# Optimization experiments

Hardware: AMD Instinct MI355X
Metric: run time of the kernel (lower is better)

The kernel has to match this reference:

```python
import jax, jax.numpy as jnp
import numpy as np

H = 1024      # hidden_size
NH = 16       # num_attention_heads
HD = H // NH  # head_size
DF = 4096     # ff intermediate
EPS = 1e-5


def layer_norm(x, g, b):
    mu = jnp.mean(x, axis=-1, keepdims=True)
    var = jnp.var(x, axis=-1, keepdims=True)
    return (x - mu) * jax.lax.rsqrt(var + EPS) * g + b


def setup_inputs() -> dict:
    key = jax.random.key(0)
    ks = jax.random.split(key, 4)
    s = 0.02
    return {
        "x": jax.random.normal(ks[0], (2, 2048, H), dtype=jnp.float32),
        "w_qkv": jax.random.normal(ks[1], (H, 3 * H), dtype=jnp.float32) * s,
        "ln1_g": jnp.ones((H,), jnp.float32),
        "ln1_b": jnp.zeros((H,), jnp.float32),
        "w1": jax.random.normal(ks[2], (H, DF), dtype=jnp.float32) * s,
        "b1": jnp.zeros((DF,), jnp.float32),
        "w2": jax.random.normal(ks[3], (DF, H), dtype=jnp.float32) * s,
        "b2": jnp.zeros((H,), jnp.float32),
        "ln2_g": jnp.ones((H,), jnp.float32),
        "ln2_b": jnp.zeros((H,), jnp.float32),
    }


def reference(x, w_qkv, ln1_g, ln1_b, w1, b1, w2, b2, ln2_g, ln2_b):
    b, s, h = x.shape
    # --- MHSelfAttention (naive) ---
    qkv = x @ w_qkv                                   # [b, s, 3h]
    qkv = qkv.reshape(b, s, 3, NH, HD)
    q, k, v = (jnp.moveaxis(qkv, 2, 0)                # [3, b, s, nh, hd]
               .transpose(0, 1, 3, 2, 4))             # [3, b, nh, s, hd]
    # NOTE: faithful quirk — scaled by sqrt(hidden_size), not head_size
    scores = jnp.einsum('bnqd,bnkd->bnqk', q, k) / jnp.sqrt(jnp.float32(h))
    probs = jax.nn.softmax(scores, axis=-1)
    ctx = jnp.einsum('bnqk,bnkd->bnqd', probs, v)     # [b, nh, s, hd]
    attn_out = ctx.transpose(0, 2, 1, 3).reshape(b, s, h)
    # post-norm residual (dropout = identity in eval)
    x = x + layer_norm(attn_out, ln1_g, ln1_b)
    # --- FFN ---
    ff = jax.nn.relu(x @ w1 + b1) @ w2 + b2
    x = x + layer_norm(ff, ln2_g, ln2_b)
    return x
```

## Files before the change

### kernel.cpp

```cpp
#include <hip/hip_runtime.h>


typedef unsigned short u16;
typedef unsigned int u32;
typedef __bf16 bf16x8 __attribute__((ext_vector_type(8)));
typedef float f32x4 __attribute__((ext_vector_type(4)));
typedef float f32x16 __attribute__((ext_vector_type(16)));
typedef u32 u32x4 __attribute__((ext_vector_type(4)));
typedef u16 u16x4 __attribute__((ext_vector_type(4)));

__device__ __forceinline__ u16 f2b(float f) {
  u32 u = __builtin_bit_cast(u32, f);
  u += 0x7fffu + ((u >> 16) & 1u);
  return (u16)(u >> 16);
}
__device__ __forceinline__ float b2f(u16 u) {
  return __builtin_bit_cast(float, (u32)u << 16);
}

__device__ __forceinline__ u32 cvtpk(float lo, float hi) {
  u32 r;
  asm("v_cvt_pk_bf16_f32 %0, %1, %2" : "=v"(r) : "v"(lo), "v"(hi));
  return r;
}

__device__ __forceinline__ void gld_lds16(const u16* g, u16* l) {
  __builtin_amdgcn_global_load_lds(
      (const __attribute__((address_space(1))) u32*)g,
      (__attribute__((address_space(3))) u32*)l, 16, 0, 0);
}

__device__ __forceinline__ void transpose32(
    const float* __restrict__ in, u16* __restrict__ out, int R, int C,
    int bx, int by, float (*tile)[33], int tid) {
  const int cb = bx * 32, rb = by * 32;
  const int c = tid & 31;
  const int r0 = tid >> 5;
#pragma unroll
  for (int rr = 0; rr < 32; rr += 8)
    tile[r0 + rr][c] = in[(size_t)(rb + r0 + rr) * C + cb + c];
  __syncthreads();
#pragma unroll
  for (int rr = 0; rr < 32; rr += 8)
    out[(size_t)(cb + r0 + rr) * R + rb + c] = f2b(tile[c][r0 + rr]);
}

__global__ __launch_bounds__(256) void prep1_kernel(
    const float* __restrict__ x, u16* __restrict__ xb,
    const float* __restrict__ w_qkv, u16* __restrict__ wqkvT) {
  __shared__ float tile[32][33];
  const int bid = blockIdx.x;
  const int tid = threadIdx.x;
  if (bid < 4096) {
    const int idx = bid * 256 + tid;
    float4 v = ((const float4*)x)[idx];
    u16x4 o = { f2b(v.x), f2b(v.y), f2b(v.z), f2b(v.w) };
    ((u16x4*)xb)[idx] = o;
  } else {
    const int t = bid - 4096;
    transpose32(w_qkv, wqkvT, 1024, 3072, t % 96, t / 96, tile, tid);
  }
}

__global__ __launch_bounds__(256) void prep2_kernel(
    const float* __restrict__ w1, u16* __restrict__ w1T,
    const float* __restrict__ w2, u16* __restrict__ w2T) {
  __shared__ float tile[32][33];
  const int bid = blockIdx.x;
  const int tid = threadIdx.x;
  if (bid < 4096) {
    transpose32(w1, w1T, 1024, 4096, bid % 128, bid / 128, tile, tid);
  } else {
    const int t = bid - 4096;
    transpose32(w2, w2T, 4096, 1024, t % 32, t / 32, tile, tid);
  }
}

__global__ __launch_bounds__(256) void transpose_v_kernel(
    const u16* __restrict__ qkv, u16* __restrict__ vt) {
  __shared__ u16 t[64][70];
  const int bh = blockIdx.x, st = blockIdx.y;
  const int b = bh >> 4, nh = bh & 15;
  const int s0 = st * 64;
  const int r = threadIdx.x >> 3, c = (threadIdx.x & 7) << 3;
  const u16* src = qkv + (size_t)(b * 2048 + s0) * 3072 + 2048 + nh * 64;
#pragma unroll
  for (int rr = 0; rr < 64; rr += 32)
    *(u32x4*)&t[r + rr][c] = *(const u32x4*)(src + (size_t)(r + rr) * 3072 + c);
  __syncthreads();
  u16* dst = vt + ((size_t)bh * 64) * 2048 + s0;
#pragma unroll
  for (int rr = 0; rr < 64; rr += 32) {
    const int d = r + rr;
    u16 tmp[8];
#pragma unroll
    for (int j = 0; j < 8; ++j) tmp[j] = t[c + j][d];
    *(u32x4*)(dst + (size_t)d * 2048 + c) = *(u32x4*)tmp;
  }
}

#define GT16(BUF, SBUF, T2, VM)                                               \
  {                                                                           \
    const u16(*Ab)[32] = As[BUF];                                             \
    const u16(*Bb)[32] = Bs[BUF];                                             \
    bf16x8 af[4], bfr[4];                                                     \
    _Pragma("unroll") for (int nr = 0; nr < 4; ++nr)                          \
        bfr[nr] = *(const bf16x8*)&Bb[wn * 64 + nr * 16 + l16][cRd];          \
    _Pragma("unroll") for (int mr = 0; mr < 4; ++mr)                          \
        af[mr] = *(const bf16x8*)&Ab[wm * 64 + mr * 16 + l16][cRd];           \
    if ((T2) >= 0) {                                                          \
      gld_lds16(Ag + (size_t)(T2) * 32, &As[SBUF][w * 16][0]);                \
      gld_lds16(Bg + (size_t)(T2) * 32, &Bs[SBUF][w * 16][0]);                \
    }                                                                         \
    asm volatile("s_waitcnt lgkmcnt(0)" ::: "memory");                        \
    __builtin_amdgcn_sched_barrier(0);                                        \
    __builtin_amdgcn_s_setprio(1);                                            \
    _Pragma("unroll") for (int mr = 0; mr < 4; ++mr)                          \
        _Pragma("unroll") for (int nr = 0; nr < 4; ++nr)                      \
            acc[mr][nr] = __builtin_amdgcn_mfma_f32_16x16x32_bf16(            \
                af[mr], bfr[nr], acc[mr][nr], 0, 0, 0);                       \
    __builtin_amdgcn_s_setprio(0);                                            \
    if ((VM) == 2) asm volatile("s_waitcnt vmcnt(2)" ::: "memory");           \
    else if ((VM) == 0) asm volatile("s_waitcnt vmcnt(0)" ::: "memory");      \
    if ((VM) >= 0) __builtin_amdgcn_s_barrier();                              \
  }

__global__ __launch_bounds__(1024) void gemm256_kernel(
    const u16* __restrict__ A, const u16* __restrict__ Bt,
    const float* __restrict__ bias, u16* __restrict__ Cb,
    int M, int N, int K, int relu,
    u16* __restrict__ Cb1, u16* __restrict__ Cb2, u16* __restrict__ Cb3) {
  const int nN = N >> 8;
  const int lin = (blockIdx.x & 7) * ((int)gridDim.x >> 3) + (blockIdx.x >> 3);
  const int m0 = (lin / nN) << 8;
  const int n0 = (lin % nN) << 8;
  const int z = blockIdx.y;
  if (z == 1) Cb = Cb1; else if (z == 2) Cb = Cb2; else if (z == 3) Cb = Cb3;

  const int tid = threadIdx.x;
  const int w = tid >> 6, lane = tid & 63;
  const int quad = lane >> 4, l16 = lane & 15;
  const int wm = w >> 2, wn = w & 3;

  __shared__ u16 As[3][256][32];
  __shared__ u16 Bs[3][256][32];

  f32x4 acc[4][4];
#pragma unroll
  for (int i = 0; i < 4; ++i)
#pragma unroll
    for (int j = 0; j < 4; ++j) acc[i][j] = {0.f, 0.f, 0.f, 0.f};

  const int srow = lane >> 2;
  const int scol = (((lane & 3) ^ (srow & 3)) << 3);
  const u16* Ag = A + (size_t)(m0 + w * 16 + srow) * K + (size_t)z * 1024 + scol;
  const u16* Bg = Bt + (size_t)(n0 + w * 16 + srow) * K + (size_t)z * 1024 + scol;

  const int cRd = ((quad ^ (l16 & 3)) << 3);

  gld_lds16(Ag,      &As[0][w * 16][0]);
  gld_lds16(Bg,      &Bs[0][w * 16][0]);
  gld_lds16(Ag + 32, &As[1][w * 16][0]);
  gld_lds16(Bg + 32, &Bs[1][w * 16][0]);
  asm volatile("s_waitcnt vmcnt(2)" ::: "memory");
  __builtin_amdgcn_s_barrier();

  for (int tt = 0; tt < 10; ++tt) {
    const int t = tt * 3;
    GT16(0, 2, t + 2, 2)
    GT16(1, 0, t + 3, 2)
    GT16(2, 1, t + 4, 2)
  }
  GT16(0, 0, -1, 0)
  GT16(1, 0, -1, -1)

#pragma unroll
  for (int mr = 0; mr < 4; ++mr) {
    const int row = m0 + wm * 64 + mr * 16 + quad * 4;
#pragma unroll
    for (int nr = 0; nr < 4; ++nr) {
      const int col = n0 + wn * 64 + nr * 16 + l16;
      const float bv = bias ? bias[col] : 0.f;
#pragma unroll
      for (int r = 0; r < 4; ++r) {
        float v = acc[mr][nr][r] + bv;
        if (relu) v = fmaxf(v, 0.f);
        Cb[(size_t)(row + r) * N + col] = f2b(v);
      }
    }
  }
}

#define QVMC                                                                  \
  if (w < 12) { asm volatile("s_waitcnt vmcnt(2)" ::: "memory"); }            \
  else        { asm volatile("s_waitcnt vmcnt(1)" ::: "memory"); }
#define QGT16(BUF, SBUF, T2, VM)                                              \
  {                                                                           \
    const u16(*Ab)[32] = As[BUF];                                             \
    const u16(*Bb)[32] = Bs[BUF];                                             \
    bf16x8 af[4], bfr[3];                                                     \
    _Pragma("unroll") for (int nr = 0; nr < 3; ++nr)                          \
        bfr[nr] = *(const bf16x8*)&Bb[wn * 48 + nr * 16 + l16][cRd];          \
    _Pragma("unroll") for (int mr = 0; mr < 4; ++mr)                          \
        af[mr] = *(const bf16x8*)&Ab[wm * 64 + mr * 16 + l16][cRd];           \
    if ((T2) >= 0) {                                                          \
      gld_lds16(Ag + (size_t)(T2) * 32, &As[SBUF][w * 16][0]);                \
      if (w < 12)                                                             \
        gld_lds16(Bg + (size_t)(T2) * 32, &Bs[SBUF][w * 16][0]);              \
    }                                                                         \
    asm volatile("s_waitcnt lgkmcnt(0)" ::: "memory");                        \
    __builtin_amdgcn_sched_barrier(0);                                        \
    __builtin_amdgcn_s_setprio(1);                                            \
    _Pragma("unroll") for (int mr = 0; mr < 4; ++mr)                          \
        _Pragma("unroll") for (int nr = 0; nr < 3; ++nr)                      \
            acc[mr][nr] = __builtin_amdgcn_mfma_f32_16x16x32_bf16(            \
                af[mr], bfr[nr], acc[mr][nr], 0, 0, 0);                       \
    __builtin_amdgcn_s_setprio(0);                                            \
    if ((VM) == 2) { QVMC }                                                   \
    else if ((VM) == 0) asm volatile("s_waitcnt vmcnt(0)" ::: "memory");      \
    if ((VM) >= 0) __builtin_amdgcn_s_barrier();                              \
  }

__global__ __launch_bounds__(1024) void gemm_qkv_kernel(
    const u16* __restrict__ A, const u16* __restrict__ Bt,
    u16* __restrict__ Cb) {
  const int K = 1024, N = 3072;
  const int lin = (blockIdx.x & 7) * 32 + (blockIdx.x >> 3);
  const int m0 = (lin >> 4) << 8;
  const int n0 = (lin & 15) * 192;

  const int tid = threadIdx.x;
  const int w = tid >> 6, lane = tid & 63;
  const int quad = lane >> 4, l16 = lane & 15;
  const int wm = w >> 2, wn = w & 3;

  __shared__ u16 As[3][256][32];
  __shared__ u16 Bs[3][192][32];

  f32x4 acc[4][3];
#pragma unroll
  for (int i = 0; i < 4; ++i)
#pragma unroll
    for (int j = 0; j < 3; ++j) acc[i][j] = {0.f, 0.f, 0.f, 0.f};

  const int srow = lane >> 2;
  const int scol = (((lane & 3) ^ (srow & 3)) << 3);
  const u16* Ag = A + (size_t)(m0 + w * 16 + srow) * K + scol;
  const u16* Bg = Bt + (size_t)(n0 + w * 16 + srow) * K + scol;

  const int cRd = ((quad ^ (l16 & 3)) << 3);

  gld_lds16(Ag,      &As[0][w * 16][0]);
  if (w < 12) gld_lds16(Bg,      &Bs[0][w * 16][0]);
  gld_lds16(Ag + 32, &As[1][w * 16][0]);
  if (w < 12) gld_lds16(Bg + 32, &Bs[1][w * 16][0]);
  QVMC
  __builtin_amdgcn_s_barrier();

  for (int tt = 0; tt < 10; ++tt) {
    const int t = tt * 3;
    QGT16(0, 2, t + 2, 2)
    QGT16(1, 0, t + 3, 2)
    QGT16(2, 1, t + 4, 2)
  }
  QGT16(0, 0, -1, 0)
  QGT16(1, 0, -1, -1)

#pragma unroll
  for (int mr = 0; mr < 4; ++mr) {
    const int row = m0 + wm * 64 + mr * 16 + quad * 4;
#pragma unroll
    for (int nr = 0; nr < 3; ++nr) {
      const int col = n0 + wn * 48 + nr * 16 + l16;
#pragma unroll
      for (int r = 0; r < 4; ++r)
        Cb[(size_t)(row + r) * N + col] = f2b(acc[mr][nr][r]);
    }
  }
}

__global__ __launch_bounds__(256, 4) void attn_kernel(
    const u16* __restrict__ qkv, const u16* __restrict__ vt,
    float* __restrict__ Op0, float* __restrict__ Op1,
    float* __restrict__ lpart) {
  const int bh = blockIdx.x;
  const int qt = blockIdx.y;
  const int kz = blockIdx.z;
  const int b = bh >> 4, nh = bh & 15;
  const int tid = threadIdx.x;
  const int w = tid >> 6, lane = tid & 63;
  const int l32 = lane & 31, hi = lane >> 5;
  const float c2 = 0.04508422f;

  __shared__ u16 KS[64][64];
  __shared__ u16 VS[64][64];

  const size_t rs = 3072;
  const u16* qbase = qkv + (size_t)b * 2048 * rs + nh * 64;
  const u16* kbase = qbase + 1024;
  const u16* vbase = vt + (size_t)bh * 64 * 2048;
  const int q0 = qt * 128;
  const int k0beg = kz * 1024;

  bf16x8 aq[4];
  {
    const u16* qrow = qbase + (size_t)(q0 + w * 32 + l32) * rs + hi * 8;
#pragma unroll
    for (int ds = 0; ds < 4; ++ds) {
      u32x4 v = *(const u32x4*)(qrow + ds * 16);
      u16 ti[8], to[8];
      *(u32x4*)ti = v;
#pragma unroll
      for (int j = 0; j < 8; ++j) to[j] = f2b(b2f(ti[j]) * c2);
      u32x4 pk = *(u32x4*)to;
      aq[ds] = __builtin_bit_cast(bf16x8, pk);
    }
  }

  f32x16 Oacc[2];
#pragma unroll
  for (int dn = 0; dn < 2; ++dn)
#pragma unroll
    for (int i = 0; i < 16; ++i) Oacc[dn][i] = 0.f;
  float ls[4] = {0.f, 0.f, 0.f, 0.f};

  const int srow = lane >> 3;
  const int scol = ((lane & 7) ^ srow) << 3;

#pragma unroll 1
  for (int t = 0; t < 16; ++t) {
    const int k0 = k0beg + t * 64;
    __syncthreads();
    gld_lds16(kbase + (size_t)(k0 + w * 16 + srow) * rs + scol,       &KS[w * 16][0]);
    gld_lds16(kbase + (size_t)(k0 + w * 16 + 8 + srow) * rs + scol,   &KS[w * 16 + 8][0]);
    gld_lds16(vbase + (size_t)(w * 16 + srow) * 2048 + k0 + scol,     &VS[w * 16][0]);
    gld_lds16(vbase + (size_t)(w * 16 + 8 + srow) * 2048 + k0 + scol, &VS[w * 16 + 8][0]);
    __syncthreads();

    f32x16 S[2];
#pragma unroll
    for (int jt = 0; jt < 2; ++jt)
#pragma unroll
      for (int i = 0; i < 16; ++i) S[jt][i] = 0.f;
#pragma unroll
    for (int jt = 0; jt < 2; ++jt) {
      const int krow = jt * 32 + l32;
#pragma unroll
      for (int ds = 0; ds < 4; ++ds) {
        bf16x8 kv = *(const bf16x8*)&KS[krow][((2 * ds + hi) ^ (krow & 7)) << 3];
        S[jt] = __builtin_amdgcn_mfma_f32_32x32x16_bf16(kv, aq[ds], S[jt], 0, 0, 0);
      }
    }

    bf16x8 pa[4];
#pragma unroll
    for (int jt = 0; jt < 2; ++jt) {
      float p[16];
#pragma unroll
      for (int r = 0; r < 16; ++r) {
        p[r] = exp2f(S[jt][r]);
        ls[r & 3] += p[r];
      }
#pragma unroll
      for (int bq = 0; bq < 2; ++bq) {
        u32 x0 = cvtpk(p[8 * bq + 0], p[8 * bq + 1]);
        u32 y0 = cvtpk(p[8 * bq + 4], p[8 * bq + 5]);
        u32 x1 = cvtpk(p[8 * bq + 2], p[8 * bq + 3]);
        u32 y1 = cvtpk(p[8 * bq + 6], p[8 * bq + 7]);
        asm("v_permlane32_swap_b32 %0, %1" : "+v"(x0), "+v"(y0));
        asm("v_permlane32_swap_b32 %0, %1" : "+v"(x1), "+v"(y1));
        u32x4 dw = {x0, x1, y0, y1};
        pa[2 * jt + bq] = __builtin_bit_cast(bf16x8, dw);
      }
    }

#pragma unroll
    for (int dn = 0; dn < 2; ++dn) {
      const int vrow = dn * 32 + l32;
#pragma unroll
      for (int ks = 0; ks < 4; ++ks) {
        bf16x8 vv = *(const bf16x8*)&VS[vrow][((2 * ks + hi) ^ (vrow & 7)) << 3];
        Oacc[dn] = __builtin_amdgcn_mfma_f32_32x32x16_bf16(pa[ks], vv, Oacc[dn], 0, 0, 0);
      }
    }
  }

  float lsum = (ls[0] + ls[1]) + (ls[2] + ls[3]);
  const float ltot = lsum + __shfl_xor(lsum, 32);

  float* opart = kz ? Op1 : Op0;
  float* obase = opart + (size_t)b * 2048 * 1024 + (size_t)nh * 64;
  float* lbase = lpart + (size_t)kz * 4096 * 16 + (size_t)b * 2048 * 16 + nh;
#pragma unroll
  for (int r = 0; r < 16; ++r) {
    const int qrow = q0 + w * 32 + (r & 3) + 8 * (r >> 2) + 4 * hi;
#pragma unroll
    for (int dn = 0; dn < 2; ++dn)
      obase[(size_t)qrow * 1024 + dn * 32 + l32] = Oacc[dn][r];
  }
  if (lane < 32) lbase[(size_t)(q0 + w * 32 + l32) * 16] = ltot;
}

__global__ __launch_bounds__(256) void ln_attn_kernel(
    const float* __restrict__ O0, const float* __restrict__ O1,
    const float* __restrict__ l0, const float* __restrict__ l1,
    const float* __restrict__ xres, const float* __restrict__ g,
    const float* __restrict__ bb, float* __restrict__ outf,
    u16* __restrict__ outb) {
  const int w = threadIdx.x >> 6, lane = threadIdx.x & 63;
  const int row = blockIdx.x * 4 + w;
  const float4* o0r = (const float4*)(O0 + (size_t)row * 1024);
  const float4* o1r = (const float4*)(O1 + (size_t)row * 1024);
  const float* lp0 = l0 + row * 16;
  const float* lp1 = l1 + row * 16;

  float4 v[4];
  float s = 0.f, s2 = 0.f;
#pragma unroll
  for (int j = 0; j < 4; ++j) {
    const int f = j * 64 + lane;
    const int head = f >> 4;
    const float inv = 1.f / (lp0[head] + lp1[head]);
    float4 a0 = o0r[f];
    float4 a1 = o1r[f];
    v[j].x = (a0.x + a1.x) * inv;
    v[j].y = (a0.y + a1.y) * inv;
    v[j].z = (a0.z + a1.z) * inv;
    v[j].w = (a0.w + a1.w) * inv;
    s  += v[j].x + v[j].y + v[j].z + v[j].w;
    s2 += v[j].x * v[j].x + v[j].y * v[j].y + v[j].z * v[j].z + v[j].w * v[j].w;
  }
#pragma unroll
  for (int off = 32; off > 0; off >>= 1) {
    s += __shfl_xor(s, off);
    s2 += __shfl_xor(s2, off);
  }
  const float mu = s * (1.f / 1024.f);
  const float var = s2 * (1.f / 1024.f) - mu * mu;
  const float rstd = rsqrtf(var + 1e-5f);

  const float4* xr4 = (const float4*)(xres + (size_t)row * 1024);
  float4* of4 = (float4*)(outf + (size_t)row * 1024);
  u16x4* ob4 = (u16x4*)(outb + (size_t)row * 1024);
#pragma unroll
  for (int j = 0; j < 4; ++j) {
    const int f = j * 64 + lane;
    float4 xr = xr4[f];
    float4 gv = ((const float4*)g)[f];
    float4 bv = ((const float4*)bb)[f];
    float4 o;
    o.x = xr.x + (v[j].x - mu) * rstd * gv.x + bv.x;
    o.y = xr.y + (v[j].y - mu) * rstd * gv.y + bv.y;
    o.z = xr.z + (v[j].z - mu) * rstd * gv.z + bv.z;
    o.w = xr.w + (v[j].w - mu) * rstd * gv.w + bv.w;
    of4[f] = o;
    u16x4 ob = { f2b(o.x), f2b(o.y), f2b(o.z), f2b(o.w) };
    ob4[f] = ob;
  }
}

__global__ __launch_bounds__(256) void ln_ffn_kernel(
    const u16* __restrict__ p0, const u16* __restrict__ p1,
    const u16* __restrict__ p2, const u16* __restrict__ p3,
    const float* __restrict__ bias, const float* __restrict__ xres,
    const float* __restrict__ g, const float* __restrict__ bb,
    float* __restrict__ outf) {
  const int w = threadIdx.x >> 6, lane = threadIdx.x & 63;
  const int row = blockIdx.x * 4 + w;
  const u16x4* p0r = (const u16x4*)(p0 + (size_t)row * 1024);
  const u16x4* p1r = (const u16x4*)(p1 + (size_t)row * 1024);
  const u16x4* p2r = (const u16x4*)(p2 + (size_t)row * 1024);
  const u16x4* p3r = (const u16x4*)(p3 + (size_t)row * 1024);

  float4 v[4];
  float s = 0.f, s2 = 0.f;
#pragma unroll
  for (int j = 0; j < 4; ++j) {
    const int f = j * 64 + lane;
    u16x4 a0 = p0r[f];
    u16x4 a1 = p1r[f];
    u16x4 a2 = p2r[f];
    u16x4 a3 = p3r[f];
    float4 bv4 = ((const float4*)bias)[f];
    v[j].x = (b2f(a0[0]) + b2f(a1[0])) + (b2f(a2[0]) + b2f(a3[0])) + bv4.x;
    v[j].y = (b2f(a0[1]) + b2f(a1[1])) + (b2f(a2[1]) + b2f(a3[1])) + bv4.y;
    v[j].z = (b2f(a0[2]) + b2f(a1[2])) + (b2f(a2[2]) + b2f(a3[2])) + bv4.z;
    v[j].w = (b2f(a0[3]) + b2f(a1[3])) + (b2f(a2[3]) + b2f(a3[3])) + bv4.w;
    s  += v[j].x + v[j].y + v[j].z + v[j].w;
    s2 += v[j].x * v[j].x + v[j].y * v[j].y + v[j].z * v[j].z + v[j].w * v[j].w;
  }
#pragma unroll
  for (int off = 32; off > 0; off >>= 1) {
    s += __shfl_xor(s, off);
    s2 += __shfl_xor(s2, off);
  }
  const float mu = s * (1.f / 1024.f);
  const float var = s2 * (1.f / 1024.f) - mu * mu;
  const float rstd = rsqrtf(var + 1e-5f);

  const float4* xr4 = (const float4*)(xres + (size_t)row * 1024);
  float4* of4 = (float4*)(outf + (size_t)row * 1024);
#pragma unroll
  for (int j = 0; j < 4; ++j) {
    const int f = j * 64 + lane;
    float4 xr = xr4[f];
    float4 gv = ((const float4*)g)[f];
    float4 bv = ((const float4*)bb)[f];
    float4 o;
    o.x = xr.x + (v[j].x - mu) * rstd * gv.x + bv.x;
    o.y = xr.y + (v[j].y - mu) * rstd * gv.y + bv.y;
    o.z = xr.z + (v[j].z - mu) * rstd * gv.z + bv.z;
    o.w = xr.w + (v[j].w - mu) * rstd * gv.w + bv.w;
    of4[f] = o;
  }
}

extern "C" void kernel_launch(void* const* d_in, const int* in_sizes, int n_in,
                              void* d_out, int out_size, void* d_ws, size_t ws_size,
                              hipStream_t stream) {
  const float* x     = (const float*)d_in[0];
  const float* w_qkv = (const float*)d_in[1];
  const float* ln1_g = (const float*)d_in[2];
  const float* ln1_b = (const float*)d_in[3];
  const float* w1    = (const float*)d_in[4];
  const float* b1    = (const float*)d_in[5];
  const float* w2    = (const float*)d_in[6];
  const float* b2    = (const float*)d_in[7];
  const float* ln2_g = (const float*)d_in[8];
  const float* ln2_b = (const float*)d_in[9];
  float* out = (float*)d_out;
  char* ws = (char*)d_ws;

  u16*   xb    = (u16*)(ws + 0);
  u16*   wqkvT = (u16*)(ws + 8388608);
  u16*   qkvb  = (u16*)(ws + 31457280);
  u16*   vT    = (u16*)(ws + 56623104);
  float* Op0   = (float*)(ws + 0);
  float* Op1   = (float*)(ws + 73400320);
  float* lp    = (float*)(ws + 90177536);
  float* x1    = (float*)(ws + 31457280);
  u16*   x1b   = (u16*)(ws + 48234496);
  u16*   w1T   = (u16*)(ws + 14680064);
  u16*   w2T   = (u16*)(ws + 23068672);
  u16*   h1    = (u16*)(ws + 56623104);
  u16*   fp0   = (u16*)(ws + 0);
  u16*   fp1   = (u16*)(ws + 8388608);
  u16*   fp2   = (u16*)(ws + 48234496);
  u16*   fp3   = (u16*)(ws + 90177536);

  prep1_kernel<<<7168, 256, 0, stream>>>(x, xb, w_qkv, wqkvT);

  gemm_qkv_kernel<<<256, 1024, 0, stream>>>(xb, wqkvT, qkvb);
  transpose_v_kernel<<<dim3(32, 32), 256, 0, stream>>>(qkvb, vT);
  attn_kernel<<<dim3(32, 16, 2), 256, 0, stream>>>(qkvb, vT, Op0, Op1, lp);

  ln_attn_kernel<<<1024, 256, 0, stream>>>(
      Op0, Op1, lp, lp + 4096 * 16, x, ln1_g, ln1_b, x1, x1b);

  prep2_kernel<<<8192, 256, 0, stream>>>(w1, w1T, w2, w2T);

  gemm256_kernel<<<dim3(256, 1), 1024, 0, stream>>>(
      x1b, w1T, b1, h1, 4096, 4096, 1024, 1,
      nullptr, nullptr, nullptr);
  gemm256_kernel<<<dim3(64, 4), 1024, 0, stream>>>(
      h1, w2T, nullptr, fp0, 4096, 1024, 4096, 0,
      fp1, fp2, fp3);

  ln_ffn_kernel<<<1024, 256, 0, stream>>>(
      fp0, fp1, fp2, fp3, b2, x1, ln2_g, ln2_b, out);
}
```

Measured before the change: 303.9 us.

## Replace split-K FFN2 GEMM with 128x128-tile full-K kernel

```diff
diff --git a/kernel.cpp b/kernel.cpp
--- a/kernel.cpp
+++ b/kernel.cpp
@@ -128,14 +128,11 @@
 __global__ __launch_bounds__(1024) void gemm256_kernel(
     const u16* __restrict__ A, const u16* __restrict__ Bt,
     const float* __restrict__ bias, u16* __restrict__ Cb,
-    int M, int N, int K, int relu,
-    u16* __restrict__ Cb1, u16* __restrict__ Cb2, u16* __restrict__ Cb3) {
+    int M, int N, int K, int relu) {
   const int nN = N >> 8;
   const int lin = (blockIdx.x & 7) * ((int)gridDim.x >> 3) + (blockIdx.x >> 3);
   const int m0 = (lin / nN) << 8;
   const int n0 = (lin % nN) << 8;
-  const int z = blockIdx.y;
-  if (z == 1) Cb = Cb1; else if (z == 2) Cb = Cb2; else if (z == 3) Cb = Cb3;
 
   const int tid = threadIdx.x;
   const int w = tid >> 6, lane = tid & 63;
@@ -153,8 +150,8 @@
 
   const int srow = lane >> 2;
   const int scol = (((lane & 3) ^ (srow & 3)) << 3);
-  const u16* Ag = A + (size_t)(m0 + w * 16 + srow) * K + (size_t)z * 1024 + scol;
-  const u16* Bg = Bt + (size_t)(n0 + w * 16 + srow) * K + (size_t)z * 1024 + scol;
+  const u16* Ag = A + (size_t)(m0 + w * 16 + srow) * K + scol;
+  const u16* Bg = Bt + (size_t)(n0 + w * 16 + srow) * K + scol;
 
   const int cRd = ((quad ^ (l16 & 3)) << 3);
 
@@ -279,6 +276,90 @@
   }
 }
 
+#define FT(BUF, SBUF, T2, VM)                                                 \
+  {                                                                           \
+    const u16(*Ab)[32] = As[BUF];                                             \
+    const u16(*Bb)[32] = Bs[BUF];                                             \
+    bf16x8 af[2], bfr[2];                                                     \
+    _Pragma("unroll") for (int nr = 0; nr < 2; ++nr)                          \
+        bfr[nr] = *(const bf16x8*)&Bb[wn * 32 + nr * 16 + l16][cRd];          \
+    _Pragma("unroll") for (int mr = 0; mr < 2; ++mr)                          \
+        af[mr] = *(const bf16x8*)&Ab[wm * 32 + mr * 16 + l16][cRd];           \
+    if ((T2) >= 0) {                                                          \
+      if (w < 8) gld_lds16(Ag + (size_t)(T2) * 32, &As[SBUF][w * 16][0]);     \
+      else       gld_lds16(Bg + (size_t)(T2) * 32, &Bs[SBUF][(w - 8) * 16][0]);\
+    }                                                                         \
+    asm volatile("s_waitcnt lgkmcnt(0)" ::: "memory");                        \
+    __builtin_amdgcn_sched_barrier(0);                                        \
+    __builtin_amdgcn_s_setprio(1);                                            \
+    _Pragma("unroll") for (int mr = 0; mr < 2; ++mr)                          \
+        _Pragma("unroll") for (int nr = 0; nr < 2; ++nr)                      \
+            acc[mr][nr] = __builtin_amdgcn_mfma_f32_16x16x32_bf16(            \
+                af[mr], bfr[nr], acc[mr][nr], 0, 0, 0);                       \
+    __builtin_amdgcn_s_setprio(0);                                            \
+    if ((VM) == 1) asm volatile("s_waitcnt vmcnt(1)" ::: "memory");           \
+    else if ((VM) == 0) asm volatile("s_waitcnt vmcnt(0)" ::: "memory");      \
+    if ((VM) >= 0) __builtin_amdgcn_s_barrier();                              \
+  }
+
+__global__ __launch_bounds__(1024, 8) void gemm_ffn2_kernel(
+    const u16* __restrict__ A, const u16* __restrict__ Bt,
+    u16* __restrict__ Cb) {
+  const int K = 4096, N = 1024;
+  const int lin = (blockIdx.x & 7) * 32 + (blockIdx.x >> 3);
+  const int m0 = (lin >> 3) * 128;
+  const int n0 = (lin & 7) * 128;
+
+  const int tid = threadIdx.x;
+  const int w = tid >> 6, lane = tid & 63;
+  const int quad = lane >> 4, l16 = lane & 15;
+  const int wm = w >> 2, wn = w & 3;
+
+  __shared__ u16 As[3][128][32];
+  __shared__ u16 Bs[3][128][32];
+
+  f32x4 acc[2][2];
+#pragma unroll
+  for (int i = 0; i < 2; ++i)
+#pragma unroll
+    for (int j = 0; j < 2; ++j) acc[i][j] = {0.f, 0.f, 0.f, 0.f};
+
+  const int srow = lane >> 2;
+  const int scol = (((lane & 3) ^ (srow & 3)) << 3);
+  const u16* Ag = A + (size_t)(m0 + (w & 7) * 16 + srow) * K + scol;
+  const u16* Bg = Bt + (size_t)(n0 + (w & 7) * 16 + srow) * K + scol;
+
+  const int cRd = ((quad ^ (l16 & 3)) << 3);
+
+  if (w < 8) gld_lds16(Ag,      &As[0][w * 16][0]);
+  else       gld_lds16(Bg,      &Bs[0][(w - 8) * 16][0]);
+  if (w < 8) gld_lds16(Ag + 32, &As[1][w * 16][0]);
+  else       gld_lds16(Bg + 32, &Bs[1][(w - 8) * 16][0]);
+  asm volatile("s_waitcnt vmcnt(1)" ::: "memory");
+  __builtin_amdgcn_s_barrier();
+
+  for (int tt = 0; tt < 42; ++tt) {
+    const int t = tt * 3;
+    FT(0, 2, t + 2, 1)
+    FT(1, 0, t + 3, 1)
+    FT(2, 1, t + 4, 1)
+  }
+  FT(0, 0, -1, 0)
+  FT(1, 0, -1, -1)
+
+#pragma unroll
+  for (int mr = 0; mr < 2; ++mr) {
+    const int row = m0 + wm * 32 + mr * 16 + quad * 4;
+#pragma unroll
+    for (int nr = 0; nr < 2; ++nr) {
+      const int col = n0 + wn * 32 + nr * 16 + l16;
+#pragma unroll
+      for (int r = 0; r < 4; ++r)
+        Cb[(size_t)(row + r) * N + col] = f2b(acc[mr][nr][r]);
+    }
+  }
+}
+
 __global__ __launch_bounds__(256, 4) void attn_kernel(
     const u16* __restrict__ qkv, const u16* __restrict__ vt,
     float* __restrict__ Op0, float* __restrict__ Op1,
@@ -460,17 +541,12 @@
 }
 
 __global__ __launch_bounds__(256) void ln_ffn_kernel(
-    const u16* __restrict__ p0, const u16* __restrict__ p1,
-    const u16* __restrict__ p2, const u16* __restrict__ p3,
-    const float* __restrict__ bias, const float* __restrict__ xres,
-    const float* __restrict__ g, const float* __restrict__ bb,
-    float* __restrict__ outf) {
+    const u16* __restrict__ p0, const float* __restrict__ bias,
+    const float* __restrict__ xres, const float* __restrict__ g,
+    const float* __restrict__ bb, float* __restrict__ outf) {
   const int w = threadIdx.x >> 6, lane = threadIdx.x & 63;
   const int row = blockIdx.x * 4 + w;
   const u16x4* p0r = (const u16x4*)(p0 + (size_t)row * 1024);
-  const u16x4* p1r = (const u16x4*)(p1 + (size_t)row * 1024);
-  const u16x4* p2r = (const u16x4*)(p2 + (size_t)row * 1024);
-  const u16x4* p3r = (const u16x4*)(p3 + (size_t)row * 1024);
 
   float4 v[4];
   float s = 0.f, s2 = 0.f;
@@ -478,14 +554,11 @@
   for (int j = 0; j < 4; ++j) {
     const int f = j * 64 + lane;
     u16x4 a0 = p0r[f];
-    u16x4 a1 = p1r[f];
-    u16x4 a2 = p2r[f];
-    u16x4 a3 = p3r[f];
     float4 bv4 = ((const float4*)bias)[f];
-    v[j].x = (b2f(a0[0]) + b2f(a1[0])) + (b2f(a2[0]) + b2f(a3[0])) + bv4.x;
-    v[j].y = (b2f(a0[1]) + b2f(a1[1])) + (b2f(a2[1]) + b2f(a3[1])) + bv4.y;
-    v[j].z = (b2f(a0[2]) + b2f(a1[2])) + (b2f(a2[2]) + b2f(a3[2])) + bv4.z;
-    v[j].w = (b2f(a0[3]) + b2f(a1[3])) + (b2f(a2[3]) + b2f(a3[3])) + bv4.w;
+    v[j].x = b2f(a0[0]) + bv4.x;
+    v[j].y = b2f(a0[1]) + bv4.y;
+    v[j].z = b2f(a0[2]) + bv4.z;
+    v[j].w = b2f(a0[3]) + bv4.w;
     s  += v[j].x + v[j].y + v[j].z + v[j].w;
     s2 += v[j].x * v[j].x + v[j].y * v[j].y + v[j].z * v[j].z + v[j].w * v[j].w;
   }
@@ -544,9 +617,6 @@
   u16*   w2T   = (u16*)(ws + 23068672);
   u16*   h1    = (u16*)(ws + 56623104);
   u16*   fp0   = (u16*)(ws + 0);
-  u16*   fp1   = (u16*)(ws + 8388608);
-  u16*   fp2   = (u16*)(ws + 48234496);
-  u16*   fp3   = (u16*)(ws + 90177536);
 
   prep1_kernel<<<7168, 256, 0, stream>>>(x, xb, w_qkv, wqkvT);
 
@@ -560,12 +630,9 @@
   prep2_kernel<<<8192, 256, 0, stream>>>(w1, w1T, w2, w2T);
 
   gemm256_kernel<<<dim3(256, 1), 1024, 0, stream>>>(
-      x1b, w1T, b1, h1, 4096, 4096, 1024, 1,
-      nullptr, nullptr, nullptr);
-  gemm256_kernel<<<dim3(64, 4), 1024, 0, stream>>>(
-      h1, w2T, nullptr, fp0, 4096, 1024, 4096, 0,
-      fp1, fp2, fp3);
+      x1b, w1T, b1, h1, 4096, 4096, 1024, 1);
+  gemm_ffn2_kernel<<<256, 1024, 0, stream>>>(h1, w2T, fp0);
 
   ln_ffn_kernel<<<1024, 256, 0, stream>>>(
-      fp0, fp1, fp2, fp3, b2, x1, ln2_g, ln2_b, out);
-}
+      fp0, b2, x1, ln2_g, ln2_b, out);
+}
```

Measured after the change: 312.2 us. +2.7%, slower.
